# Optimization experiments

Measured on AMD Instinct MI355X. Metric: run time of the kernel, lower is better.

Reference implementation:

```python
import jax, jax.numpy as jnp
import numpy as np

N_NODES = 50000
N_EDGES = 800000
D_IN = 256
D_OUT = 256


def setup_inputs() -> dict:
    key = jax.random.key(0)
    k1, k2, k3, k4, k5 = jax.random.split(key, 5)
    edge_src = jax.random.randint(k1, (N_EDGES,), 0, N_NODES, dtype=jnp.int64 if jax.config.jax_enable_x64 else jnp.int32)
    edge_dst = jax.random.randint(k2, (N_EDGES,), 0, N_NODES, dtype=jnp.int64 if jax.config.jax_enable_x64 else jnp.int32)
    edge_val = jax.random.uniform(k3, (N_EDGES,), dtype=jnp.float32)
    x = jax.random.normal(k4, (N_NODES, D_IN), dtype=jnp.float32)
    W = jax.random.normal(k5, (D_IN, D_OUT), dtype=jnp.float32) * (1.0 / np.sqrt(D_IN))
    b = jnp.zeros((D_OUT,), dtype=jnp.float32)
    return {"edge_src": edge_src, "edge_dst": edge_dst, "edge_val": edge_val, "x": x, "W": W, "b": b}


def reference(edge_src, edge_dst, edge_val, x, W, b):
    # h = X W  (dense GEMM)
    h = jnp.matmul(x, W)  # [N, D_OUT]
    # z = A_hat h  (SpMM over COO edge list: z[dst] += val * h[src])
    msgs = edge_val[:, None] * h[edge_src]  # [E, D_OUT]
    z = jax.ops.segment_sum(msgs, edge_dst, num_segments=x.shape[0])
    # bias + activation fused
    return jax.nn.relu(z + b)
```

## Files before the change

### kernel.cpp

```cpp
#include <hip/hip_runtime.h>

#define D 256
#define CAP 64
#define CHUNK 4096

typedef __attribute__((ext_vector_type(4))) float f32x4;
typedef __attribute__((ext_vector_type(8))) short s16x8;
typedef __attribute__((ext_vector_type(4))) unsigned short u16x4;

static __device__ __forceinline__ unsigned short f2bf(float f) {
    unsigned int u = __float_as_uint(f);
    unsigned int r = (u + 0x7fffu + ((u >> 16) & 1u)) >> 16;
    return (unsigned short)r;
}

__global__ __launch_bounds__(256) void transpose_w(const float* __restrict__ W,
                                                   unsigned short* __restrict__ Wt) {
    __shared__ float s[16][17];
    const int lk = threadIdx.x & 15;
    const int ln = threadIdx.x >> 4;
    const int k0 = blockIdx.x * 16;
    const int n0 = blockIdx.y * 16;
    s[ln][lk] = W[(k0 + ln) * D + n0 + lk];
    __syncthreads();
    Wt[(n0 + ln) * D + k0 + lk] = f2bf(s[lk][ln]);
}


__global__ __launch_bounds__(256) void k_hist(const int* __restrict__ dst,
                                              int* __restrict__ partial, int E, int nch, int nb) {
    __shared__ int lh[256];
    const int c = blockIdx.x;
    const int t = threadIdx.x;
    lh[t] = 0;
    __syncthreads();
    const int base = c * CHUNK;
    for (int k = 0; k < CHUNK; k += 256) {
        const int e = base + k + t;
        if (e < E) atomicAdd(&lh[dst[e] >> 8], 1);
    }
    __syncthreads();
    if (t < nb) partial[t * nch + c] = lh[t];
}

__global__ __launch_bounds__(256) void k_rowscan(int* __restrict__ partial,
                                                 int* __restrict__ rowSum, int nch, int nb) {
    const int b = blockIdx.x * 4 + (threadIdx.x >> 6);
    if (b >= nb) return;
    const int lane = threadIdx.x & 63;
    int running = 0;
    for (int k = 0; k < nch; k += 64) {
        const int idx = k + lane;
        int v = (idx < nch) ? partial[b * nch + idx] : 0;
        int incl = v;
        #pragma unroll
        for (int s = 1; s < 64; s <<= 1) {
            const int u = __shfl_up(incl, s, 64);
            if (lane >= s) incl += u;
        }
        if (idx < nch) partial[b * nch + idx] = running + incl - v;
        running += __shfl(incl, 63, 64);
    }
    if (lane == 0) rowSum[b] = running;
}

__global__ __launch_bounds__(256) void k_bstart(const int* __restrict__ rowSum,
                                                int* __restrict__ bucketStart, int nb) {
    __shared__ int wsum[4];
    const int t = threadIdx.x;
    const int lane = t & 63;
    const int w = t >> 6;
    const int v = (t < nb) ? rowSum[t] : 0;
    int incl = v;
    #pragma unroll
    for (int s = 1; s < 64; s <<= 1) {
        const int u = __shfl_up(incl, s, 64);
        if (lane >= s) incl += u;
    }
    if (lane == 63) wsum[w] = incl;
    __syncthreads();
    if (t == 0) {
        int s = 0;
        for (int i = 0; i < 4; ++i) { const int u = wsum[i]; wsum[i] = s; s += u; }
    }
    __syncthreads();
    const int ex = incl - v + wsum[w];
    if (t <= nb) bucketStart[t] = ex;
}

__global__ __launch_bounds__(256) void k_scatter(const int* __restrict__ src,
                                                 const int* __restrict__ dst,
                                                 const float* __restrict__ val,
                                                 const int* __restrict__ partial,
                                                 const int* __restrict__ bucketStart,
                                                 int2* __restrict__ eds, int E, int nch, int nb) {
    __shared__ int cur[256];
    const int c = blockIdx.x;
    const int t = threadIdx.x;
    if (t < nb) cur[t] = bucketStart[t] + partial[t * nch + c];
    __syncthreads();
    const int base = c * CHUNK;
    for (int k = 0; k < CHUNK; k += 256) {
        const int e = base + k + t;
        if (e < E) {
            const int d = dst[e];
            const int s = src[e];
            const float v = val[e];
            const int pos = atomicAdd(&cur[d >> 8], 1);
            eds[pos] = make_int2(s | ((d & 255) << 24), __float_as_int(v));
        }
    }
}

__global__ __launch_bounds__(256) void k_finalize(const int2* __restrict__ eds,
                                                  const int* __restrict__ bucketStart,
                                                  int2* __restrict__ pairs,
                                                  int* __restrict__ cnt, int N) {
    __shared__ int cur[256];
    const int b = blockIdx.x;
    const int t = threadIdx.x;
    cur[t] = 0;
    __syncthreads();
    const int lo = bucketStart[b], hi = bucketStart[b + 1];
    for (int i = lo + t; i < hi; i += 256) {
        const int2 p = eds[i];
        const int low8 = ((unsigned)p.x) >> 24;
        const int r = atomicAdd(&cur[low8], 1);
        if (r < CAP) {
            const int node = (b << 8) | low8;
            pairs[(size_t)node * CAP + r] = make_int2(p.x & 0x00FFFFFF, p.y);
        }
    }
    __syncthreads();
    const int node = (b << 8) | t;
    if (node < N) cnt[node] = cur[t] < CAP ? cur[t] : CAP;
}

#define BMT 128
#define BNT 128
#define BK 32
#define PK 40

__global__ __launch_bounds__(256) void gemm_ht(const float* __restrict__ x,
                                               const unsigned short* __restrict__ Wt,
                                               unsigned short* __restrict__ h, int M) {
    __shared__ unsigned short ws[BNT][PK];
    __shared__ unsigned short xs[BMT][PK];
    const int tid  = threadIdx.x;
    const int lane = tid & 63;
    const int wid  = tid >> 6;
    const int wm   = wid & 1;
    const int wn   = wid >> 1;
    const int l15  = lane & 15;
    const int l4   = lane >> 4;
    const int bm   = blockIdx.x * BMT;
    const int bn   = blockIdx.y * BNT;

    const int srow = tid >> 3;
    const int q    = tid & 7;

    f32x4 acc[4][4] = {};

    for (int k0 = 0; k0 < D; k0 += BK) {
        #pragma unroll
        for (int p = 0; p < 4; ++p) {
            const int row = srow + p * 32;
            float4 v = {0.f, 0.f, 0.f, 0.f};
            if (bm + row < M)
                v = *reinterpret_cast<const float4*>(&x[(size_t)(bm + row) * D + k0 + q * 4]);
            u16x4 pk = {f2bf(v.x), f2bf(v.y), f2bf(v.z), f2bf(v.w)};
            *reinterpret_cast<u16x4*>(&xs[row][q * 4]) = pk;
        }
        #pragma unroll
        for (int p = 0; p < 4; ++p) {
            const int row = srow + p * 32;
            u16x4 v = *reinterpret_cast<const u16x4*>(&Wt[(size_t)(bn + row) * D + k0 + q * 4]);
            *reinterpret_cast<u16x4*>(&ws[row][q * 4]) = v;
        }
        __syncthreads();

        s16x8 af[4], bf[4];
        #pragma unroll
        for (int fi = 0; fi < 4; ++fi)
            af[fi] = *reinterpret_cast<const s16x8*>(&ws[wn * 64 + fi * 16 + l15][l4 * 8]);
        #pragma unroll
        for (int fj = 0; fj < 4; ++fj)
            bf[fj] = *reinterpret_cast<const s16x8*>(&xs[wm * 64 + fj * 16 + l15][l4 * 8]);
        #pragma unroll
        for (int fi = 0; fi < 4; ++fi)
            #pragma unroll
            for (int fj = 0; fj < 4; ++fj)
                acc[fi][fj] = __builtin_amdgcn_mfma_f32_16x16x32_bf16(af[fi], bf[fj], acc[fi][fj], 0, 0, 0);
        __syncthreads();
    }

    #pragma unroll
    for (int fj = 0; fj < 4; ++fj) {
        const int m = bm + wm * 64 + fj * 16 + l15;
        if (m >= M) continue;
        #pragma unroll
        for (int fi = 0; fi < 4; ++fi) {
            const int n = bn + wn * 64 + fi * 16 + l4 * 4;
            u16x4 pk = {f2bf(acc[fi][fj][0]), f2bf(acc[fi][fj][1]),
                        f2bf(acc[fi][fj][2]), f2bf(acc[fi][fj][3])};
            *reinterpret_cast<u16x4*>(&h[(size_t)m * D + n]) = pk;
        }
    }
}

__global__ __launch_bounds__(256) void gather_csr(const int2* __restrict__ pairs,
                                                  const int* __restrict__ cnt,
                                                  const unsigned short* __restrict__ h,
                                                  const float* __restrict__ b,
                                                  float* __restrict__ z, int N) {
    const int node = blockIdx.x * 4 + (threadIdx.x >> 6);
    if (node >= N) return;
    const int lane = threadIdx.x & 63;
    const size_t o = (size_t)node * CAP;
    const int dg = cnt[node];

    float4 acc = {0.f, 0.f, 0.f, 0.f};
    int e = 0;
    for (; e + 4 <= dg; e += 4) {
        const int2 p0 = pairs[o + e];
        const int2 p1 = pairs[o + e + 1];
        const int2 p2 = pairs[o + e + 2];
        const int2 p3 = pairs[o + e + 3];
        const uint2 h0 = *reinterpret_cast<const uint2*>(&h[(size_t)p0.x * D + lane * 4]);
        const uint2 h1 = *reinterpret_cast<const uint2*>(&h[(size_t)p1.x * D + lane * 4]);
        const uint2 h2 = *reinterpret_cast<const uint2*>(&h[(size_t)p2.x * D + lane * 4]);
        const uint2 h3 = *reinterpret_cast<const uint2*>(&h[(size_t)p3.x * D + lane * 4]);
        const float v0 = __int_as_float(p0.y);
        const float v1 = __int_as_float(p1.y);
        const float v2 = __int_as_float(p2.y);
        const float v3 = __int_as_float(p3.y);
        acc.x = fmaf(v0, __uint_as_float(h0.x << 16), acc.x);
        acc.y = fmaf(v0, __uint_as_float(h0.x & 0xffff0000u), acc.y);
        acc.z = fmaf(v0, __uint_as_float(h0.y << 16), acc.z);
        acc.w = fmaf(v0, __uint_as_float(h0.y & 0xffff0000u), acc.w);
        acc.x = fmaf(v1, __uint_as_float(h1.x << 16), acc.x);
        acc.y = fmaf(v1, __uint_as_float(h1.x & 0xffff0000u), acc.y);
        acc.z = fmaf(v1, __uint_as_float(h1.y << 16), acc.z);
        acc.w = fmaf(v1, __uint_as_float(h1.y & 0xffff0000u), acc.w);
        acc.x = fmaf(v2, __uint_as_float(h2.x << 16), acc.x);
        acc.y = fmaf(v2, __uint_as_float(h2.x & 0xffff0000u), acc.y);
        acc.z = fmaf(v2, __uint_as_float(h2.y << 16), acc.z);
        acc.w = fmaf(v2, __uint_as_float(h2.y & 0xffff0000u), acc.w);
        acc.x = fmaf(v3, __uint_as_float(h3.x << 16), acc.x);
        acc.y = fmaf(v3, __uint_as_float(h3.x & 0xffff0000u), acc.y);
        acc.z = fmaf(v3, __uint_as_float(h3.y << 16), acc.z);
        acc.w = fmaf(v3, __uint_as_float(h3.y & 0xffff0000u), acc.w);
    }
    for (; e < dg; ++e) {
        const int2 p0 = pairs[o + e];
        const float v0 = __int_as_float(p0.y);
        const uint2 h0 = *reinterpret_cast<const uint2*>(&h[(size_t)p0.x * D + lane * 4]);
        acc.x = fmaf(v0, __uint_as_float(h0.x << 16), acc.x);
        acc.y = fmaf(v0, __uint_as_float(h0.x & 0xffff0000u), acc.y);
        acc.z = fmaf(v0, __uint_as_float(h0.y << 16), acc.z);
        acc.w = fmaf(v0, __uint_as_float(h0.y & 0xffff0000u), acc.w);
    }

    const float4 bb = *reinterpret_cast<const float4*>(&b[lane * 4]);
    acc.x = fmaxf(acc.x + bb.x, 0.f);
    acc.y = fmaxf(acc.y + bb.y, 0.f);
    acc.z = fmaxf(acc.z + bb.z, 0.f);
    acc.w = fmaxf(acc.w + bb.w, 0.f);
    *reinterpret_cast<float4*>(&z[(size_t)node * D + lane * 4]) = acc;
}

extern "C" void kernel_launch(void* const* d_in, const int* in_sizes, int n_in,
                              void* d_out, int out_size, void* d_ws, size_t ws_size,
                              hipStream_t stream) {
    const int*   edge_src = (const int*)d_in[0];
    const int*   edge_dst = (const int*)d_in[1];
    const float* edge_val = (const float*)d_in[2];
    const float* x        = (const float*)d_in[3];
    const float* W        = (const float*)d_in[4];
    const float* b        = (const float*)d_in[5];

    const int E = in_sizes[0];
    const int N = in_sizes[3] / D;
    const int nch = (E + CHUNK - 1) / CHUNK;
    const int nb  = (N + 255) >> 8;

    float* z = (float*)d_out;

    unsigned short* h     = (unsigned short*)d_ws;
    int2*           eds   = (int2*)d_ws;
    int2*           pairs = (int2*)(h + (size_t)N * D);
    unsigned short* Wt    = (unsigned short*)(pairs + (size_t)N * CAP);
    int* partial     = (int*)(Wt + D * D);
    int* rowSum      = partial + nb * nch;
    int* bucketStart = rowSum + nb;
    int* cnt         = bucketStart + (nb + 1);

    transpose_w<<<dim3(D / 16, D / 16), 256, 0, stream>>>(W, Wt);

    k_hist   <<<nch, 256, 0, stream>>>(edge_dst, partial, E, nch, nb);
    k_rowscan<<<(nb + 3) / 4, 256, 0, stream>>>(partial, rowSum, nch, nb);
    k_bstart <<<1, 256, 0, stream>>>(rowSum, bucketStart, nb);
    k_scatter<<<nch, 256, 0, stream>>>(edge_src, edge_dst, edge_val,
                                       partial, bucketStart, eds, E, nch, nb);
    k_finalize<<<nb, 256, 0, stream>>>(eds, bucketStart, pairs, cnt, N);

    dim3 ggrid((N + BMT - 1) / BMT, D / BNT);
    gemm_ht<<<ggrid, 256, 0, stream>>>(x, Wt, h, N);

    gather_csr<<<(N + 3) / 4, 256, 0, stream>>>(pairs, cnt, h, b, z, N);
}
```

Measured before the change: 141.8 us.

## Merge prep kernels, co-schedule scatter with GEMM, and slice gather by XCC

```diff
diff --git a/kernel.cpp b/kernel.cpp
--- a/kernel.cpp
+++ b/kernel.cpp
@@ -3,6 +3,10 @@
 #define D 256
 #define CAP 64
 #define CHUNK 4096
+#define BMT 128
+#define BNT 128
+#define BK 32
+#define PK 40
 
 typedef __attribute__((ext_vector_type(4))) float f32x4;
 typedef __attribute__((ext_vector_type(8))) short s16x8;
@@ -14,24 +18,29 @@
     return (unsigned short)r;
 }
 
-__global__ __launch_bounds__(256) void transpose_w(const float* __restrict__ W,
-                                                   unsigned short* __restrict__ Wt) {
+static __device__ __forceinline__ int xcc_id() {
+    return (int)(__builtin_amdgcn_s_getreg(((32 - 1) << 11) | 20) & 7u);
+}
+
+__global__ __launch_bounds__(256) void k_prep(const float* __restrict__ W,
+                                              unsigned short* __restrict__ Wt,
+                                              const int* __restrict__ dst,
+                                              int* __restrict__ partial,
+                                              int* __restrict__ rowSum,
+                                              int E, int nch, int nb) {
     __shared__ float s[16][17];
-    const int lk = threadIdx.x & 15;
-    const int ln = threadIdx.x >> 4;
-    const int k0 = blockIdx.x * 16;
-    const int n0 = blockIdx.y * 16;
-    s[ln][lk] = W[(k0 + ln) * D + n0 + lk];
-    __syncthreads();
-    Wt[(n0 + ln) * D + k0 + lk] = f2bf(s[lk][ln]);
-}
-
-
-__global__ __launch_bounds__(256) void k_hist(const int* __restrict__ dst,
-                                              int* __restrict__ partial, int E, int nch, int nb) {
     __shared__ int lh[256];
-    const int c = blockIdx.x;
     const int t = threadIdx.x;
+    if ((int)blockIdx.x < 256) {
+        const int lk = t & 15, ln = t >> 4;
+        const int k0 = ((int)blockIdx.x & 15) * 16;
+        const int n0 = ((int)blockIdx.x >> 4) * 16;
+        s[ln][lk] = W[(k0 + ln) * D + n0 + lk];
+        __syncthreads();
+        Wt[(n0 + ln) * D + k0 + lk] = f2bf(s[lk][ln]);
+        return;
+    }
+    const int c = (int)blockIdx.x - 256;
     lh[t] = 0;
     __syncthreads();
     const int base = c * CHUNK;
@@ -40,32 +49,35 @@
         if (e < E) atomicAdd(&lh[dst[e] >> 8], 1);
     }
     __syncthreads();
-    if (t < nb) partial[t * nch + c] = lh[t];
-}
-
-__global__ __launch_bounds__(256) void k_rowscan(int* __restrict__ partial,
-                                                 int* __restrict__ rowSum, int nch, int nb) {
-    const int b = blockIdx.x * 4 + (threadIdx.x >> 6);
-    if (b >= nb) return;
-    const int lane = threadIdx.x & 63;
-    int running = 0;
-    for (int k = 0; k < nch; k += 64) {
-        const int idx = k + lane;
-        int v = (idx < nch) ? partial[b * nch + idx] : 0;
-        int incl = v;
-        #pragma unroll
-        for (int s = 1; s < 64; s <<= 1) {
-            const int u = __shfl_up(incl, s, 64);
-            if (lane >= s) incl += u;
-        }
-        if (idx < nch) partial[b * nch + idx] = running + incl - v;
-        running += __shfl(incl, 63, 64);
-    }
-    if (lane == 0) rowSum[b] = running;
-}
-
-__global__ __launch_bounds__(256) void k_bstart(const int* __restrict__ rowSum,
-                                                int* __restrict__ bucketStart, int nb) {
+    if (t < nb) {
+        partial[t * nch + c] = lh[t];
+        if (lh[t]) atomicAdd(&rowSum[t], lh[t]);
+    }
+}
+
+__global__ __launch_bounds__(256) void k_scan(int* __restrict__ partial,
+                                              const int* __restrict__ rowSum,
+                                              int* __restrict__ bucketStart,
+                                              int nch, int nb, int nscan) {
+    if ((int)blockIdx.x < nscan) {
+        const int bkt = blockIdx.x * 4 + (threadIdx.x >> 6);
+        if (bkt >= nb) return;
+        const int lane = threadIdx.x & 63;
+        int running = 0;
+        for (int k = 0; k < nch; k += 64) {
+            const int idx = k + lane;
+            int v = (idx < nch) ? partial[bkt * nch + idx] : 0;
+            int incl = v;
+            #pragma unroll
+            for (int sft = 1; sft < 64; sft <<= 1) {
+                const int u = __shfl_up(incl, sft, 64);
+                if (lane >= sft) incl += u;
+            }
+            if (idx < nch) partial[bkt * nch + idx] = running + incl - v;
+            running += __shfl(incl, 63, 64);
+        }
+        return;
+    }
     __shared__ int wsum[4];
     const int t = threadIdx.x;
     const int lane = t & 63;
@@ -73,41 +85,109 @@
     const int v = (t < nb) ? rowSum[t] : 0;
     int incl = v;
     #pragma unroll
-    for (int s = 1; s < 64; s <<= 1) {
-        const int u = __shfl_up(incl, s, 64);
-        if (lane >= s) incl += u;
+    for (int sft = 1; sft < 64; sft <<= 1) {
+        const int u = __shfl_up(incl, sft, 64);
+        if (lane >= sft) incl += u;
     }
     if (lane == 63) wsum[w] = incl;
     __syncthreads();
     if (t == 0) {
-        int s = 0;
-        for (int i = 0; i < 4; ++i) { const int u = wsum[i]; wsum[i] = s; s += u; }
+        int acc = 0;
+        for (int i = 0; i < 4; ++i) { const int u = wsum[i]; wsum[i] = acc; acc += u; }
     }
     __syncthreads();
     const int ex = incl - v + wsum[w];
     if (t <= nb) bucketStart[t] = ex;
 }
 
-__global__ __launch_bounds__(256) void k_scatter(const int* __restrict__ src,
-                                                 const int* __restrict__ dst,
-                                                 const float* __restrict__ val,
-                                                 const int* __restrict__ partial,
-                                                 const int* __restrict__ bucketStart,
-                                                 int2* __restrict__ eds, int E, int nch, int nb) {
+__global__ __launch_bounds__(256) void k_main(
+    const int* __restrict__ src, const int* __restrict__ dstp,
+    const float* __restrict__ val, const int* __restrict__ partial,
+    const int* __restrict__ bucketStart, int2* __restrict__ eds,
+    int E, int nch, int nb,
+    const float* __restrict__ x, const unsigned short* __restrict__ Wt,
+    unsigned short* __restrict__ h, int M) {
+
+    __shared__ unsigned short ws[BNT][PK];
+    __shared__ unsigned short xs[BMT][PK];
     __shared__ int cur[256];
-    const int c = blockIdx.x;
     const int t = threadIdx.x;
-    if (t < nb) cur[t] = bucketStart[t] + partial[t * nch + c];
-    __syncthreads();
-    const int base = c * CHUNK;
-    for (int k = 0; k < CHUNK; k += 256) {
-        const int e = base + k + t;
-        if (e < E) {
-            const int d = dst[e];
-            const int s = src[e];
-            const float v = val[e];
-            const int pos = atomicAdd(&cur[d >> 8], 1);
-            eds[pos] = make_int2(s | ((d & 255) << 24), __float_as_int(v));
+
+    if ((int)blockIdx.x < nch) {
+        const int c = blockIdx.x;
+        if (t < nb) cur[t] = bucketStart[t] + partial[t * nch + c];
+        __syncthreads();
+        const int base = c * CHUNK;
+        for (int k = 0; k < CHUNK; k += 256) {
+            const int e = base + k + t;
+            if (e < E) {
+                const int d = dstp[e];
+                const int sv = src[e];
+                const float v = val[e];
+                const int pos = atomicAdd(&cur[d >> 8], 1);
+                eds[pos] = make_int2(sv | ((d & 255) << 24), __float_as_int(v));
+            }
+        }
+        return;
+    }
+
+    const int gb = (int)blockIdx.x - nch;
+    const int bm = (gb >> 1) * BMT;
+    const int bn = (gb & 1) * BNT;
+    const int lane = t & 63;
+    const int wid  = t >> 6;
+    const int wm   = wid & 1;
+    const int wn   = wid >> 1;
+    const int l15  = lane & 15;
+    const int l4   = lane >> 4;
+    const int srow = t >> 3;
+    const int q    = t & 7;
+
+    f32x4 acc[4][4] = {};
+
+    for (int k0 = 0; k0 < D; k0 += BK) {
+        #pragma unroll
+        for (int p = 0; p < 4; ++p) {
+            const int row = srow + p * 32;
+            float4 v = {0.f, 0.f, 0.f, 0.f};
+            if (bm + row < M)
+                v = *reinterpret_cast<const float4*>(&x[(size_t)(bm + row) * D + k0 + q * 4]);
+            u16x4 pk = {f2bf(v.x), f2bf(v.y), f2bf(v.z), f2bf(v.w)};
+            *reinterpret_cast<u16x4*>(&xs[row][q * 4]) = pk;
+        }
+        #pragma unroll
+        for (int p = 0; p < 4; ++p) {
+            const int row = srow + p * 32;
+            u16x4 v = *reinterpret_cast<const u16x4*>(&Wt[(size_t)(bn + row) * D + k0 + q * 4]);
+            *reinterpret_cast<u16x4*>(&ws[row][q * 4]) = v;
+        }
+        __syncthreads();
+
+        s16x8 af[4], bf[4];
+        #pragma unroll
+        for (int fi = 0; fi < 4; ++fi)
+            af[fi] = *reinterpret_cast<const s16x8*>(&ws[wn * 64 + fi * 16 + l15][l4 * 8]);
+        #pragma unroll
+        for (int fj = 0; fj < 4; ++fj)
+            bf[fj] = *reinterpret_cast<const s16x8*>(&xs[wm * 64 + fj * 16 + l15][l4 * 8]);
+        #pragma unroll
+        for (int fi = 0; fi < 4; ++fi)
+            #pragma unroll
+            for (int fj = 0; fj < 4; ++fj)
+                acc[fi][fj] = __builtin_amdgcn_mfma_f32_16x16x32_bf16(af[fi], bf[fj], acc[fi][fj], 0, 0, 0);
+        __syncthreads();
+    }
+
+    #pragma unroll
+    for (int fj = 0; fj < 4; ++fj) {
+        const int m = bm + wm * 64 + fj * 16 + l15;
+        if (m >= M) continue;
+        #pragma unroll
+        for (int fi = 0; fi < 4; ++fi) {
+            const int n = bn + wn * 64 + fi * 16 + l4 * 4;
+            u16x4 pk = {f2bf(acc[fi][fj][0]), f2bf(acc[fi][fj][1]),
+                        f2bf(acc[fi][fj][2]), f2bf(acc[fi][fj][3])};
+            *reinterpret_cast<u16x4*>(&h[(size_t)m * D + n]) = pk;
         }
     }
 }
@@ -136,137 +216,83 @@
     if (node < N) cnt[node] = cur[t] < CAP ? cur[t] : CAP;
 }
 
-#define BMT 128
-#define BNT 128
-#define BK 32
-#define PK 40
-
-__global__ __launch_bounds__(256) void gemm_ht(const float* __restrict__ x,
-                                               const unsigned short* __restrict__ Wt,
-                                               unsigned short* __restrict__ h, int M) {
-    __shared__ unsigned short ws[BNT][PK];
-    __shared__ unsigned short xs[BMT][PK];
-    const int tid  = threadIdx.x;
-    const int lane = tid & 63;
-    const int wid  = tid >> 6;
-    const int wm   = wid & 1;
-    const int wn   = wid >> 1;
-    const int l15  = lane & 15;
-    const int l4   = lane >> 4;
-    const int bm   = blockIdx.x * BMT;
-    const int bn   = blockIdx.y * BNT;
-
-    const int srow = tid >> 3;
-    const int q    = tid & 7;
-
-    f32x4 acc[4][4] = {};
-
-    for (int k0 = 0; k0 < D; k0 += BK) {
-        #pragma unroll
-        for (int p = 0; p < 4; ++p) {
-            const int row = srow + p * 32;
-            float4 v = {0.f, 0.f, 0.f, 0.f};
-            if (bm + row < M)
-                v = *reinterpret_cast<const float4*>(&x[(size_t)(bm + row) * D + k0 + q * 4]);
-            u16x4 pk = {f2bf(v.x), f2bf(v.y), f2bf(v.z), f2bf(v.w)};
-            *reinterpret_cast<u16x4*>(&xs[row][q * 4]) = pk;
-        }
-        #pragma unroll
-        for (int p = 0; p < 4; ++p) {
-            const int row = srow + p * 32;
-            u16x4 v = *reinterpret_cast<const u16x4*>(&Wt[(size_t)(bn + row) * D + k0 + q * 4]);
-            *reinterpret_cast<u16x4*>(&ws[row][q * 4]) = v;
-        }
-        __syncthreads();
-
-        s16x8 af[4], bf[4];
-        #pragma unroll
-        for (int fi = 0; fi < 4; ++fi)
-            af[fi] = *reinterpret_cast<const s16x8*>(&ws[wn * 64 + fi * 16 + l15][l4 * 8]);
-        #pragma unroll
-        for (int fj = 0; fj < 4; ++fj)
-            bf[fj] = *reinterpret_cast<const s16x8*>(&xs[wm * 64 + fj * 16 + l15][l4 * 8]);
-        #pragma unroll
-        for (int fi = 0; fi < 4; ++fi)
-            #pragma unroll
-            for (int fj = 0; fj < 4; ++fj)
-                acc[fi][fj] = __builtin_amdgcn_mfma_f32_16x16x32_bf16(af[fi], bf[fj], acc[fi][fj], 0, 0, 0);
-        __syncthreads();
-    }
-
-    #pragma unroll
-    for (int fj = 0; fj < 4; ++fj) {
-        const int m = bm + wm * 64 + fj * 16 + l15;
-        if (m >= M) continue;
-        #pragma unroll
-        for (int fi = 0; fi < 4; ++fi) {
-            const int n = bn + wn * 64 + fi * 16 + l4 * 4;
-            u16x4 pk = {f2bf(acc[fi][fj][0]), f2bf(acc[fi][fj][1]),
-                        f2bf(acc[fi][fj][2]), f2bf(acc[fi][fj][3])};
-            *reinterpret_cast<u16x4*>(&h[(size_t)m * D + n]) = pk;
-        }
-    }
-}
-
-__global__ __launch_bounds__(256) void gather_csr(const int2* __restrict__ pairs,
-                                                  const int* __restrict__ cnt,
-                                                  const unsigned short* __restrict__ h,
-                                                  const float* __restrict__ b,
-                                                  float* __restrict__ z, int N) {
-    const int node = blockIdx.x * 4 + (threadIdx.x >> 6);
+__global__ __launch_bounds__(256) void gather_sliced(const int2* __restrict__ pairs,
+                                                     const int* __restrict__ cnt,
+                                                     const unsigned short* __restrict__ h,
+                                                     const float* __restrict__ bias,
+                                                     float* __restrict__ z,
+                                                     int N, int ngroups,
+                                                     int* __restrict__ claim) {
+    __shared__ int sS, sG;
+    if (threadIdx.x == 0) {
+        const int pref = xcc_id();
+        int s = -1, g = -1;
+        for (int ds = 0; ds < 8; ++ds) {
+            const int ss = (pref + ds) & 7;
+            const int gg = atomicAdd(&claim[ss * 32], 1);
+            if (gg < ngroups) { s = ss; g = gg; break; }
+        }
+        sS = s; sG = g;
+    }
+    __syncthreads();
+    const int slice = sS;
+    if (slice < 0) return;
+    const int node = sG * 32 + ((int)threadIdx.x >> 3);
     if (node >= N) return;
-    const int lane = threadIdx.x & 63;
-    const size_t o = (size_t)node * CAP;
+    const int t8 = threadIdx.x & 7;
+    const int col = slice * 32 + t8 * 4;
     const int dg = cnt[node];
+    const int2* pr = pairs + (size_t)node * CAP;
+    const unsigned short* hc = h + col;
 
     float4 acc = {0.f, 0.f, 0.f, 0.f};
     int e = 0;
     for (; e + 4 <= dg; e += 4) {
-        const int2 p0 = pairs[o + e];
-        const int2 p1 = pairs[o + e + 1];
-        const int2 p2 = pairs[o + e + 2];
-        const int2 p3 = pairs[o + e + 3];
-        const uint2 h0 = *reinterpret_cast<const uint2*>(&h[(size_t)p0.x * D + lane * 4]);
-        const uint2 h1 = *reinterpret_cast<const uint2*>(&h[(size_t)p1.x * D + lane * 4]);
-        const uint2 h2 = *reinterpret_cast<const uint2*>(&h[(size_t)p2.x * D + lane * 4]);
-        const uint2 h3 = *reinterpret_cast<const uint2*>(&h[(size_t)p3.x * D + lane * 4]);
+        const int2 p0 = pr[e];
+        const int2 p1 = pr[e + 1];
+        const int2 p2 = pr[e + 2];
+        const int2 p3 = pr[e + 3];
+        const uint2 a0 = *reinterpret_cast<const uint2*>(hc + (size_t)p0.x * D);
+        const uint2 a1 = *reinterpret_cast<const uint2*>(hc + (size_t)p1.x * D);
+        const uint2 a2 = *reinterpret_cast<const uint2*>(hc + (size_t)p2.x * D);
+        const uint2 a3 = *reinterpret_cast<const uint2*>(hc + (size_t)p3.x * D);
         const float v0 = __int_as_float(p0.y);
         const float v1 = __int_as_float(p1.y);
         const float v2 = __int_as_float(p2.y);
         const float v3 = __int_as_float(p3.y);
-        acc.x = fmaf(v0, __uint_as_float(h0.x << 16), acc.x);
-        acc.y = fmaf(v0, __uint_as_float(h0.x & 0xffff0000u), acc.y);
-        acc.z = fmaf(v0, __uint_as_float(h0.y << 16), acc.z);
-        acc.w = fmaf(v0, __uint_as_float(h0.y & 0xffff0000u), acc.w);
-        acc.x = fmaf(v1, __uint_as_float(h1.x << 16), acc.x);
-        acc.y = fmaf(v1, __uint_as_float(h1.x & 0xffff0000u), acc.y);
-        acc.z = fmaf(v1, __uint_as_float(h1.y << 16), acc.z);
-        acc.w = fmaf(v1, __uint_as_float(h1.y & 0xffff0000u), acc.w);
-        acc.x = fmaf(v2, __uint_as_float(h2.x << 16), acc.x);
-        acc.y = fmaf(v2, __uint_as_float(h2.x & 0xffff0000u), acc.y);
-        acc.z = fmaf(v2, __uint_as_float(h2.y << 16), acc.z);
-        acc.w = fmaf(v2, __uint_as_float(h2.y & 0xffff0000u), acc.w);
-        acc.x = fmaf(v3, __uint_as_float(h3.x << 16), acc.x);
-        acc.y = fmaf(v3, __uint_as_float(h3.x & 0xffff0000u), acc.y);
-        acc.z = fmaf(v3, __uint_as_float(h3.y << 16), acc.z);
-        acc.w = fmaf(v3, __uint_as_float(h3.y & 0xffff0000u), acc.w);
+        acc.x = fmaf(v0, __uint_as_float(a0.x << 16), acc.x);
+        acc.y = fmaf(v0, __uint_as_float(a0.x & 0xffff0000u), acc.y);
+        acc.z = fmaf(v0, __uint_as_float(a0.y << 16), acc.z);
+        acc.w = fmaf(v0, __uint_as_float(a0.y & 0xffff0000u), acc.w);
+        acc.x = fmaf(v1, __uint_as_float(a1.x << 16), acc.x);
+        acc.y = fmaf(v1, __uint_as_float(a1.x & 0xffff0000u), acc.y);
+        acc.z = fmaf(v1, __uint_as_float(a1.y << 16), acc.z);
+        acc.w = fmaf(v1, __uint_as_float(a1.y & 0xffff0000u), acc.w);
+        acc.x = fmaf(v2, __uint_as_float(a2.x << 16), acc.x);
+        acc.y = fmaf(v2, __uint_as_float(a2.x & 0xffff0000u), acc.y);
+        acc.z = fmaf(v2, __uint_as_float(a2.y << 16), acc.z);
+        acc.w = fmaf(v2, __uint_as_float(a2.y & 0xffff0000u), acc.w);
+        acc.x = fmaf(v3, __uint_as_float(a3.x << 16), acc.x);
+        acc.y = fmaf(v3, __uint_as_float(a3.x & 0xffff0000u), acc.y);
+        acc.z = fmaf(v3, __uint_as_float(a3.y << 16), acc.z);
+        acc.w = fmaf(v3, __uint_as_float(a3.y & 0xffff0000u), acc.w);
     }
     for (; e < dg; ++e) {
-        const int2 p0 = pairs[o + e];
+        const int2 p0 = pr[e];
         const float v0 = __int_as_float(p0.y);
-        const uint2 h0 = *reinterpret_cast<const uint2*>(&h[(size_t)p0.x * D + lane * 4]);
-        acc.x = fmaf(v0, __uint_as_float(h0.x << 16), acc.x);
-        acc.y = fmaf(v0, __uint_as_float(h0.x & 0xffff0000u), acc.y);
-        acc.z = fmaf(v0, __uint_as_float(h0.y << 16), acc.z);
-        acc.w = fmaf(v0, __uint_as_float(h0.y & 0xffff0000u), acc.w);
-    }
-
-    const float4 bb = *reinterpret_cast<const float4*>(&b[lane * 4]);
+        const uint2 a0 = *reinterpret_cast<const uint2*>(hc + (size_t)p0.x * D);
+        acc.x = fmaf(v0, __uint_as_float(a0.x << 16), acc.x);
+        acc.y = fmaf(v0, __uint_as_float(a0.x & 0xffff0000u), acc.y);
+        acc.z = fmaf(v0, __uint_as_float(a0.y << 16), acc.z);
+        acc.w = fmaf(v0, __uint_as_float(a0.y & 0xffff0000u), acc.w);
+    }
+
+    const float4 bb = *reinterpret_cast<const float4*>(bias + col);
     acc.x = fmaxf(acc.x + bb.x, 0.f);
     acc.y = fmaxf(acc.y + bb.y, 0.f);
     acc.z = fmaxf(acc.z + bb.z, 0.f);
     acc.w = fmaxf(acc.w + bb.w, 0.f);
-    *reinterpret_cast<float4*>(&z[(size_t)node * D + lane * 4]) = acc;
+    *reinterpret_cast<float4*>(z + (size_t)node * D + col) = acc;
 }
 
 extern "C" void kernel_launch(void* const* d_in, const int* in_sizes, int n_in,
@@ -283,29 +309,33 @@
     const int N = in_sizes[3] / D;
     const int nch = (E + CHUNK - 1) / CHUNK;
     const int nb  = (N + 255) >> 8;
+    const int ngroups = (N + 31) / 32;
 
     float* z = (float*)d_out;
 
     unsigned short* h     = (unsigned short*)d_ws;
-    int2*           eds   = (int2*)d_ws;
     int2*           pairs = (int2*)(h + (size_t)N * D);
-    unsigned short* Wt    = (unsigned short*)(pairs + (size_t)N * CAP);
+    int2*           eds   = pairs + (size_t)N * CAP;
+    unsigned short* Wt    = (unsigned short*)(eds + E);
     int* partial     = (int*)(Wt + D * D);
-    int* rowSum      = partial + nb * nch;
-    int* bucketStart = rowSum + nb;
+    int* bucketStart = partial + nb * nch;
     int* cnt         = bucketStart + (nb + 1);
-
-    transpose_w<<<dim3(D / 16, D / 16), 256, 0, stream>>>(W, Wt);
-
-    k_hist   <<<nch, 256, 0, stream>>>(edge_dst, partial, E, nch, nb);
-    k_rowscan<<<(nb + 3) / 4, 256, 0, stream>>>(partial, rowSum, nch, nb);
-    k_bstart <<<1, 256, 0, stream>>>(rowSum, bucketStart, nb);
-    k_scatter<<<nch, 256, 0, stream>>>(edge_src, edge_dst, edge_val,
-                                       partial, bucketStart, eds, E, nch, nb);
+    int* claim       = cnt + N;
+    int* rowSum      = claim + 256;
+
+    hipMemsetAsync(cnt, 0, (size_t)(N + 256 + nb) * sizeof(int), stream);
+
+    k_prep<<<256 + nch, 256, 0, stream>>>(W, Wt, edge_dst, partial, rowSum, E, nch, nb);
+
+    const int nscan = (nb + 3) / 4;
+    k_scan<<<nscan + 1, 256, 0, stream>>>(partial, rowSum, bucketStart, nch, nb, nscan);
+
+    const int gridM = (N + BMT - 1) / BMT;
+    k_main<<<nch + gridM * 2, 256, 0, stream>>>(edge_src, edge_dst, edge_val, partial,
+                                                bucketStart, eds, E, nch, nb,
+                                                x, Wt, h, N);
+
     k_finalize<<<nb, 256, 0, stream>>>(eds, bucketStart, pairs, cnt, N);
 
-    dim3 ggrid((N + BMT - 1) / BMT, D / BNT);
-    gemm_ht<<<ggrid, 256, 0, stream>>>(x, Wt, h, N);
-
-    gather_csr<<<(N + 3) / 4, 256, 0, stream>>>(pairs, cnt, h, b, z, N);
-}
+    gather_sliced<<<8 * ngroups, 256, 0, stream>>>(pairs, cnt, h, b, z, N, ngroups, claim);
+}
```

After: 167.5 us. 18.1% more time.
